# Optimization experiments

Measured on AMD Instinct MI355X. Metric: run time of the kernel, lower is better.

The kernel has to match this reference:

```python
import jax, jax.numpy as jnp
import numpy as np

UNITS = 1024
N_FEATURES = 128
OUT_STEPS = 32
EPS = 1e-7


def _lstm_cell(x, h, c, W, U, b):
    # Keras LSTMCell: gates ordered i, f, g(candidate), o
    z = x @ W + h @ U + b  # [B, 4U]
    i, f, g, o = jnp.split(z, 4, axis=-1)
    i = jax.nn.sigmoid(i)
    f = jax.nn.sigmoid(f)
    g = jnp.tanh(g)
    o = jax.nn.sigmoid(o)
    c_new = f * c + i * g
    h_new = o * jnp.tanh(c_new)
    return h_new, c_new


def setup_inputs() -> dict:
    key = jax.random.key(0)
    ks = jax.random.split(key, 12)
    B, T, F, U = 512, 64, N_FEATURES, UNITS
    s = lambda fan_in: 1.0 / np.sqrt(fan_in)
    return {
        "inputs": jax.random.normal(ks[0], (B, T, F), jnp.float32),
        "mean": jax.random.normal(ks[1], (F,), jnp.float32) * 0.1,
        "var": jax.random.uniform(ks[2], (F,), jnp.float32, 0.5, 1.5),
        "W1": jax.random.normal(ks[3], (F, 4 * U), jnp.float32) * s(F),
        "U1": jax.random.normal(ks[4], (U, 4 * U), jnp.float32) * s(U),
        "b1": jnp.zeros((4 * U,), jnp.float32),
        "W2": jax.random.normal(ks[5], (U, 4 * U), jnp.float32) * s(U),
        "U2": jax.random.normal(ks[6], (U, 4 * U), jnp.float32) * s(U),
        "b2": jnp.zeros((4 * U,), jnp.float32),
        "Wd": jax.random.normal(ks[7], (U, F), jnp.float32) * s(U),
        "bd": jnp.zeros((F,), jnp.float32),
    }


def reference(inputs, mean, var, W1, U1, b1, W2, U2, b2, Wd, bd):
    B = inputs.shape[0]
    inv_std = jax.lax.rsqrt(var + EPS)
    # NOTE: original call() normalizes, then warmup() normalizes AGAIN -- faithful.
    x = (inputs - mean) * inv_std
    x = (x - mean) * inv_std

    # --- warmup: RNN(cell1) over input sequence, return last h and state ---
    h0 = jnp.zeros((B, UNITS), x.dtype)
    c0 = jnp.zeros((B, UNITS), x.dtype)

    def warm_step(carry, xt):
        h, c = carry
        h, c = _lstm_cell(xt, h, c, W1, U1, b1)
        return (h, c), None

    (h, c), _ = jax.lax.scan(warm_step, (h0, c0), jnp.swapaxes(x, 0, 1))
    pred0 = h @ Wd + bd  # [B, F]

    def ar_step(carry, _):
        pred, h, c = carry
        h, c = _lstm_cell(pred, h, c, W1, U1, b1)
        h, c = _lstm_cell(h, h, c, W2, U2, b2)
        pred = h @ Wd + bd
        return (pred, h, c), pred

    _, preds = jax.lax.scan(ar_step, (pred0, h, c), None, length=OUT_STEPS - 1)
    preds = jnp.concatenate([pred0[None], preds], axis=0)  # [out_steps, B, F]
    return jnp.transpose(preds, (1, 0, 2))  # [B, out_steps, F]
```

## Files before the change

kernel.cpp:

```cpp
#include <hip/hip_runtime.h>
#include <stdint.h>

#define NB 512
#define NT 64
#define NF 128
#define NU 1024
#define NG 4096
#define NS 32

typedef __attribute__((ext_vector_type(8))) short short8;
typedef __attribute__((ext_vector_type(4))) float f32x4;
typedef __attribute__((ext_vector_type(4))) unsigned int u32x4;

__device__ __forceinline__ float sigm(float x) { return 1.0f / (1.0f + __expf(-x)); }
__device__ __forceinline__ float tanh_f(float x) {
  float ax = fabsf(x);
  float e = __expf(2.0f * ax);
  float t = 1.0f - 2.0f / (e + 1.0f);
  return copysignf(t, x);
}
__device__ __forceinline__ unsigned short f2bf(float f) {
  union { float f; unsigned u; } v; v.f = f;
  unsigned r = v.u + 0x7fffu + ((v.u >> 16) & 1u);
  return (unsigned short)(r >> 16);
}

__device__ __forceinline__ void coh_store_bf16(unsigned short* p, unsigned v) {
  asm volatile("global_store_short %0, %1, off sc0 sc1" :: "v"(p), "v"(v) : "memory");
}

__device__ __forceinline__ void gbar_grp(unsigned* gf, int u_blk, unsigned gen) {
  __syncthreads();
  if (threadIdx.x == 0)
    __hip_atomic_store(gf + u_blk, gen, __ATOMIC_RELAXED, __HIP_MEMORY_SCOPE_AGENT);
  if (threadIdx.x < 16) {
    while (__hip_atomic_load(gf + threadIdx.x, __ATOMIC_RELAXED, __HIP_MEMORY_SCOPE_AGENT) < gen)
      __builtin_amdgcn_s_sleep(1);
  }
  __syncthreads();
}

template <int KX>
__device__ __forceinline__ void do_step(
    const unsigned short* __restrict__ hIn,
    const unsigned short* __restrict__ Bp,
    const unsigned short* __restrict__ Xp,
    const unsigned short* __restrict__ W1p,
    int tstep, f32x4 bA, f32x4 (&cst)[2],
    unsigned short* __restrict__ hOut, unsigned short* __restrict__ hOut2,
    unsigned short* lds,
    int r0, int u0, int kh, int wu, int lr, int g4, int ucol, int tid)
{
  constexpr int ROWE = NU + KX;

  {
    u32x4 t[8];
    const unsigned short* src[8];
    int loff[8];
#pragma unroll
    for (int it = 0; it < 8; ++it) {
      int i = tid + it * 512;
      int r = i >> 7, cb = i & 127;
      src[it] = hIn + (size_t)(r0 + r) * NU + cb * 8;
      loff[it] = r * (ROWE * 2) + ((cb * 16) ^ ((r & 7) << 4));
    }
#pragma unroll
    for (int it = 0; it < 8; ++it)
      asm volatile("global_load_dwordx4 %0, %1, off sc0 sc1" : "=v"(t[it]) : "v"(src[it]));
    if constexpr (KX > 0) {
      int r = tid >> 4, cb = tid & 15;
      u32x4 vx = *(const u32x4*)(Xp + ((size_t)tstep * NB + (r0 + r)) * NF + cb * 8);
      int ox = r * (ROWE * 2) + ((NU * 2 + cb * 16) ^ ((r & 7) << 4));
      asm volatile("s_waitcnt vmcnt(0)" ::: "memory");
      __builtin_amdgcn_sched_barrier(0);
#pragma unroll
      for (int it = 0; it < 8; ++it) *(u32x4*)((char*)lds + loff[it]) = t[it];
      *(u32x4*)((char*)lds + ox) = vx;
    } else {
      asm volatile("s_waitcnt vmcnt(0)" ::: "memory");
      __builtin_amdgcn_sched_barrier(0);
#pragma unroll
      for (int it = 0; it < 8; ++it) *(u32x4*)((char*)lds + loff[it]) = t[it];
    }
  }
  __syncthreads();

  f32x4 acc[4][2];
#pragma unroll
  for (int g = 0; g < 4; ++g)
#pragma unroll
    for (int rt = 0; rt < 2; ++rt) acc[g][rt] = (f32x4){0.f, 0.f, 0.f, 0.f};

  const char* ldsb = (const char*)lds;
  const int arow0 = lr * (ROWE * 2);
  const int arow1 = (16 + lr) * (ROWE * 2);
  const int axor = (lr & 7) << 4;
  const int kcb = kh * 16;

  short8 nb[2][4];
  {
    size_t b0 = ((size_t)(kcb * 4 + g4) * NG + ucol) * 8;
    size_t b1 = ((size_t)((kcb + 1) * 4 + g4) * NG + ucol) * 8;
#pragma unroll
    for (int g = 0; g < 4; ++g) {
      nb[0][g] = *(const short8*)(Bp + b0 + (size_t)g * NU * 8);
      nb[1][g] = *(const short8*)(Bp + b1 + (size_t)g * NU * 8);
    }
  }
#pragma unroll 4
  for (int kc = 0; kc < 16; ++kc) {
    short8 bb[4];
#pragma unroll
    for (int g = 0; g < 4; ++g) bb[g] = nb[kc & 1][g];
    if (kc < 14) {
      size_t base = ((size_t)((kcb + kc + 2) * 4 + g4) * NG + ucol) * 8;
#pragma unroll
      for (int g = 0; g < 4; ++g) nb[kc & 1][g] = *(const short8*)(Bp + base + (size_t)g * NU * 8);
    }
    int kb = ((kcb + kc) * 64 + g4 * 16) ^ axor;
    short8 a0 = *(const short8*)(ldsb + arow0 + kb);
    short8 a1 = *(const short8*)(ldsb + arow1 + kb);
#pragma unroll
    for (int g = 0; g < 4; ++g) {
      acc[g][0] = __builtin_amdgcn_mfma_f32_16x16x32_bf16(a0, bb[g], acc[g][0], 0, 0, 0);
      acc[g][1] = __builtin_amdgcn_mfma_f32_16x16x32_bf16(a1, bb[g], acc[g][1], 0, 0, 0);
    }
  }
  if constexpr (KX > 0) {
#pragma unroll
    for (int kc = kh * 2; kc < kh * 2 + 2; ++kc) {
      int kb = (NU * 2 + kc * 64 + g4 * 16) ^ axor;
      short8 a0 = *(const short8*)(ldsb + arow0 + kb);
      short8 a1 = *(const short8*)(ldsb + arow1 + kb);
      size_t base = ((size_t)(kc * 4 + g4) * NG + ucol) * 8;
      short8 bb[4];
#pragma unroll
      for (int g = 0; g < 4; ++g) bb[g] = *(const short8*)(W1p + base + (size_t)g * NU * 8);
#pragma unroll
      for (int g = 0; g < 4; ++g) {
        acc[g][0] = __builtin_amdgcn_mfma_f32_16x16x32_bf16(a0, bb[g], acc[g][0], 0, 0, 0);
        acc[g][1] = __builtin_amdgcn_mfma_f32_16x16x32_bf16(a1, bb[g], acc[g][1], 0, 0, 0);
      }
    }
  }

  __syncthreads();
  float* red = (float*)lds;
  const int l = (g4 << 4) | lr;
  if (kh == 1) {
#pragma unroll
    for (int g = 0; g < 4; ++g)
#pragma unroll
      for (int rt = 0; rt < 2; ++rt)
        *(f32x4*)(red + (size_t)(((wu * 8) + (g * 2 + rt)) * 64 + l) * 4) = acc[g][rt];
  }
  __syncthreads();
  if (kh == 0) {
#pragma unroll
    for (int g = 0; g < 4; ++g)
#pragma unroll
      for (int rt = 0; rt < 2; ++rt)
        acc[g][rt] += *(const f32x4*)(red + (size_t)(((wu * 8) + (g * 2 + rt)) * 64 + l) * 4);

#pragma unroll
    for (int rt = 0; rt < 2; ++rt) {
#pragma unroll
      for (int j = 0; j < 4; ++j) {
        int r = r0 + rt * 16 + g4 * 4 + j;
        size_t idx = (size_t)r * NU + ucol;
        float iv = sigm(acc[0][rt][j] + bA[0]);
        float fv = sigm(acc[1][rt][j] + bA[1]);
        float gv = tanh_f(acc[2][rt][j] + bA[2]);
        float ov = sigm(acc[3][rt][j] + bA[3]);
        float cN = fv * cst[rt][j] + iv * gv;
        cst[rt][j] = cN;
        unsigned hv = f2bf(ov * tanh_f(cN));
        coh_store_bf16(hOut + idx, hv);
        if (hOut2) coh_store_bf16(hOut2 + idx, hv);
      }
    }
  }
}

__global__ __launch_bounds__(512, 2) void lstm_seq(
    const unsigned short* __restrict__ U1p, const unsigned short* __restrict__ U1pp,
    const unsigned short* __restrict__ W2U2p, const unsigned short* __restrict__ W1p,
    const unsigned short* __restrict__ x2,
    const float* __restrict__ b1, const float* __restrict__ b1p, const float* __restrict__ b2,
    unsigned short* __restrict__ h0, unsigned short* __restrict__ h1,
    unsigned short* __restrict__ hist, unsigned* __restrict__ flags)
{
  extern __shared__ unsigned short lds[];
  const int bid = blockIdx.x;
  const int xcd = bid & 7, slot = bid >> 3;
  const int u_blk = xcd * 2 + (slot >> 4);
  const int m_blk = slot & 15;
  const int r0 = m_blk * 32, u0 = u_blk * 64;
  const int tid = threadIdx.x;
  const int w = tid >> 6, kh = w >> 2, wu = w & 3;
  const int lr = tid & 15, g4 = (tid >> 4) & 3;
  const int ucol = u0 + wu * 16 + lr;
  const size_t HS = (size_t)NB * NU;
  unsigned* gf = flags + m_blk * 64;

  f32x4 bW, bC1, bC2;
#pragma unroll
  for (int g = 0; g < 4; ++g) {
    bW[g]  = b1 [g * NU + ucol];
    bC1[g] = b1p[g * NU + ucol];
    bC2[g] = b2 [g * NU + ucol];
  }
  f32x4 cst[2];
  cst[0] = (f32x4){0.f, 0.f, 0.f, 0.f};
  cst[1] = (f32x4){0.f, 0.f, 0.f, 0.f};

  unsigned gen = 0;
  for (int t = 0; t < NT; ++t) {
    const unsigned short* hi = (t & 1) ? h1 : h0;
    unsigned short* ho = (t & 1) ? h0 : h1;
    do_step<NF>(hi, U1p, x2, W1p, t, bW, cst, ho, (t == NT - 1) ? hist : nullptr,
                lds, r0, u0, kh, wu, lr, g4, ucol, tid);
    gbar_grp(gf, u_blk, ++gen);
  }
  for (int s = 0; s < NS - 1; ++s) {
    do_step<0>(h0, U1pp, nullptr, nullptr, 0, bC1, cst, h1, nullptr,
               lds, r0, u0, kh, wu, lr, g4, ucol, tid);
    gbar_grp(gf, u_blk, ++gen);
    do_step<0>(h1, W2U2p, nullptr, nullptr, 0, bC2, cst, h0, hist + (size_t)(s + 1) * HS,
               lds, r0, u0, kh, wu, lr, g4, ucol, tid);
    if (s < NS - 2) gbar_grp(gf, u_blk, ++gen);
  }
}

__global__ __launch_bounds__(256, 2) void pred_gemm(
    const unsigned short* __restrict__ H,
    const unsigned short* __restrict__ Wdp,
    const float* __restrict__ bd, float* __restrict__ out)
{
  __shared__ unsigned short lds[32 * NU];
  const int tid = threadIdx.x;
  const int r0 = blockIdx.x * 32;
  for (int i = tid; i < 32 * 128; i += 256) {
    int r = i >> 7, cb = i & 127;
    uint4 v = *(const uint4*)(H + (size_t)(r0 + r) * NU + cb * 8);
    int off = r * 2048 + ((cb * 16) ^ ((r & 7) << 4));
    *(uint4*)((char*)lds + off) = v;
  }
  __syncthreads();
  const int w = tid >> 6, l = tid & 63, lr = l & 15, g4 = l >> 4;
  f32x4 acc[2][2];
#pragma unroll
  for (int a = 0; a < 2; ++a)
#pragma unroll
    for (int c = 0; c < 2; ++c) acc[a][c] = (f32x4){0.f, 0.f, 0.f, 0.f};
  const char* ldsb = (const char*)lds;
  const int arow0 = lr * 2048, arow1 = (16 + lr) * 2048, axor = (lr & 7) << 4;
  const int col0 = w * 32 + lr;
#pragma unroll 4
  for (int kc = 0; kc < 32; ++kc) {
    int kb = (kc * 64 + g4 * 16) ^ axor;
    short8 a0 = *(const short8*)(ldsb + arow0 + kb);
    short8 a1 = *(const short8*)(ldsb + arow1 + kb);
    size_t base = ((size_t)(kc * 4 + g4) * NF) * 8;
    short8 w0 = *(const short8*)(Wdp + base + (size_t)col0 * 8);
    short8 w1 = *(const short8*)(Wdp + base + (size_t)(col0 + 16) * 8);
    acc[0][0] = __builtin_amdgcn_mfma_f32_16x16x32_bf16(a0, w0, acc[0][0], 0, 0, 0);
    acc[1][0] = __builtin_amdgcn_mfma_f32_16x16x32_bf16(a1, w0, acc[1][0], 0, 0, 0);
    acc[0][1] = __builtin_amdgcn_mfma_f32_16x16x32_bf16(a0, w1, acc[0][1], 0, 0, 0);
    acc[1][1] = __builtin_amdgcn_mfma_f32_16x16x32_bf16(a1, w1, acc[1][1], 0, 0, 0);
  }
#pragma unroll
  for (int rt = 0; rt < 2; ++rt)
#pragma unroll
    for (int ct = 0; ct < 2; ++ct)
#pragma unroll
      for (int j = 0; j < 4; ++j) {
        int r = r0 + rt * 16 + g4 * 4 + j;
        int s = r >> 9, bb = r & 511;
        int f = w * 32 + ct * 16 + lr;
        out[((size_t)bb * NS + s) * NF + f] = acc[rt][ct][j] + bd[f];
      }
}

__global__ void prep_x(const float* __restrict__ in, const float* __restrict__ mean,
                       const float* __restrict__ var, unsigned short* __restrict__ x2) {
  int i = (blockIdx.x * 256 + threadIdx.x) * 4;
  int f = i & 127;
  int bt = i >> 7;
  int b = bt >> 6, t = bt & 63;
  float4 v = *(const float4*)(in + i);
  float vv[4] = {v.x, v.y, v.z, v.w};
  unsigned short o[4] __attribute__((aligned(8)));
#pragma unroll
  for (int j = 0; j < 4; ++j) {
    float inv = rsqrtf(var[f + j] + 1e-7f);
    float s = inv * inv;
    float m2 = mean[f + j] * (s + inv);
    o[j] = f2bf(vv[j] * s - m2);
  }
  *(uint2*)(x2 + (((size_t)t * NB + b) << 7) + f) = *(const uint2*)o;
}

__global__ void prep_pack(const float* __restrict__ A, const float* __restrict__ A2,
                          unsigned short* __restrict__ P, int N) {
  int idx = blockIdx.x * 256 + threadIdx.x;
  int kg = idx / N, c = idx - kg * N;
  unsigned short o[8] __attribute__((aligned(16)));
#pragma unroll
  for (int j = 0; j < 8; ++j) {
    size_t e = (size_t)(kg * 8 + j) * N + c;
    float vv = A[e];
    if (A2) vv += A2[e];
    o[j] = f2bf(vv);
  }
  *(uint4*)(P + (size_t)idx * 8) = *(const uint4*)o;
}

__global__ __launch_bounds__(256) void prep_u1pp(
    const float* __restrict__ U1, const float* __restrict__ Wd,
    const float* __restrict__ W1, unsigned short* __restrict__ P) {
  __shared__ float wd[8][NF];
  const int kg = blockIdx.x >> 4;
  const int c = ((blockIdx.x & 15) << 8) + threadIdx.x;
  for (int i = threadIdx.x; i < 8 * NF; i += 256)
    wd[i >> 7][i & 127] = Wd[(size_t)(kg * 8 + (i >> 7)) * NF + (i & 127)];
  __syncthreads();
  float a[8];
#pragma unroll
  for (int j = 0; j < 8; ++j) a[j] = U1[(size_t)(kg * 8 + j) * NG + c];
#pragma unroll 8
  for (int m = 0; m < NF; ++m) {
    float w1v = W1[(size_t)m * NG + c];
#pragma unroll
    for (int j = 0; j < 8; ++j) a[j] += wd[j][m] * w1v;
  }
  unsigned short o[8] __attribute__((aligned(16)));
#pragma unroll
  for (int j = 0; j < 8; ++j) o[j] = f2bf(a[j]);
  *(uint4*)(P + (size_t)(kg * NG + c) * 8) = *(const uint4*)o;
}

__global__ void prep_wdp(const float* __restrict__ Wd, unsigned short* __restrict__ P) {
  int idx = blockIdx.x * 256 + threadIdx.x;
  int kg = idx >> 7, f = idx & 127;
  unsigned short o[8] __attribute__((aligned(16)));
#pragma unroll
  for (int j = 0; j < 8; ++j) o[j] = f2bf(Wd[(size_t)(kg * 8 + j) * NF + f]);
  *(uint4*)(P + (size_t)idx * 8) = *(const uint4*)o;
}

__global__ void prep_b1p(const float* __restrict__ b1, const float* __restrict__ bd,
                         const float* __restrict__ W1, float* __restrict__ o) {
  int c = blockIdx.x * 256 + threadIdx.x;
  float acc = b1[c];
#pragma unroll 8
  for (int m = 0; m < NF; ++m) acc += bd[m] * W1[(size_t)m * NG + c];
  o[c] = acc;
}

extern "C" void kernel_launch(void* const* d_in, const int* in_sizes, int n_in,
                              void* d_out, int out_size, void* d_ws, size_t ws_size,
                              hipStream_t stream) {
  const float* inputs = (const float*)d_in[0];
  const float* mean = (const float*)d_in[1];
  const float* var  = (const float*)d_in[2];
  const float* W1   = (const float*)d_in[3];
  const float* U1   = (const float*)d_in[4];
  const float* b1   = (const float*)d_in[5];
  const float* W2   = (const float*)d_in[6];
  const float* U2   = (const float*)d_in[7];
  const float* b2   = (const float*)d_in[8];
  const float* Wd   = (const float*)d_in[9];
  const float* bd   = (const float*)d_in[10];
  float* out = (float*)d_out;
  char* ws = (char*)d_ws;

  size_t off = 0;
  auto alloc = [&](size_t bytes) { char* p = ws + off; off += (bytes + 255) & ~255ull; return p; };
  unsigned short* h0    = (unsigned short*)alloc((size_t)NB * NU * 2);
  unsigned short* h1    = (unsigned short*)alloc((size_t)NB * NU * 2);
  unsigned short* hist  = (unsigned short*)alloc((size_t)NS * NB * NU * 2);
  unsigned short* x2    = (unsigned short*)alloc((size_t)NB * NT * NF * 2);
  unsigned short* U1p   = (unsigned short*)alloc((size_t)NU * NG * 2);
  unsigned short* U1pp  = (unsigned short*)alloc((size_t)NU * NG * 2);
  unsigned short* W2U2p = (unsigned short*)alloc((size_t)NU * NG * 2);
  unsigned short* W1p   = (unsigned short*)alloc((size_t)NF * NG * 2);
  unsigned short* Wdp   = (unsigned short*)alloc((size_t)NU * NF * 2);
  float* b1p            = (float*)alloc((size_t)NG * 4);
  unsigned* flags       = (unsigned*)alloc(16 * 64 * 4);

  hipMemsetAsync(h0, 0, (size_t)NB * NU * 2, stream);
  hipMemsetAsync(flags, 0, 16 * 64 * 4, stream);

  prep_x   <<<(NB * NT * NF) / 1024, 256, 0, stream>>>(inputs, mean, var, x2);
  prep_pack<<<(NU / 8) * NG / 256, 256, 0, stream>>>(U1, nullptr, U1p, NG);
  prep_u1pp<<<(NU / 8) * NG / 256, 256, 0, stream>>>(U1, Wd, W1, U1pp);
  prep_pack<<<(NU / 8) * NG / 256, 256, 0, stream>>>(W2, U2, W2U2p, NG);
  prep_pack<<<(NF / 8) * NG / 256, 256, 0, stream>>>(W1, nullptr, W1p, NG);
  prep_wdp <<<(NU / 8) * NF / 256, 256, 0, stream>>>(Wd, Wdp);
  prep_b1p <<<NG / 256, 256, 0, stream>>>(b1, bd, W1, b1p);

  lstm_seq<<<256, 512, 98304, stream>>>(U1p, U1pp, W2U2p, W1p, x2,
                                        b1, b1p, b2, h0, h1, hist, flags);

  pred_gemm<<<(NS * NB) / 32, 256, 0, stream>>>(hist, Wdp, bd, out);
}
```

Before: 1.208 ms.

## Split grid barrier so weight prefetch overlaps the wait for peers

The group barrier is split into a signal at the end of each step and a wait at the start of the next. The first six k-chunks of recurrent weights, which do not depend on other blocks, are issued before spinning on peer flags, so weight fetch latency hides behind synchronisation. The weight prefetch ring also grows from double-buffered to six-deep with a fully unrolled k loop. The cost is higher register pressure, and the spin now sits after outstanding loads.

```diff
diff --git a/kernel.cpp b/kernel.cpp
--- a/kernel.cpp
+++ b/kernel.cpp
@@ -24,20 +24,10 @@
   unsigned r = v.u + 0x7fffu + ((v.u >> 16) & 1u);
   return (unsigned short)(r >> 16);
 }
+__device__ __forceinline__ short8 as_s8(u32x4 v) { return __builtin_bit_cast(short8, v); }
 
 __device__ __forceinline__ void coh_store_bf16(unsigned short* p, unsigned v) {
   asm volatile("global_store_short %0, %1, off sc0 sc1" :: "v"(p), "v"(v) : "memory");
-}
-
-__device__ __forceinline__ void gbar_grp(unsigned* gf, int u_blk, unsigned gen) {
-  __syncthreads();
-  if (threadIdx.x == 0)
-    __hip_atomic_store(gf + u_blk, gen, __ATOMIC_RELAXED, __HIP_MEMORY_SCOPE_AGENT);
-  if (threadIdx.x < 16) {
-    while (__hip_atomic_load(gf + threadIdx.x, __ATOMIC_RELAXED, __HIP_MEMORY_SCOPE_AGENT) < gen)
-      __builtin_amdgcn_s_sleep(1);
-  }
-  __syncthreads();
 }
 
 template <int KX>
@@ -49,9 +39,28 @@
     int tstep, f32x4 bA, f32x4 (&cst)[2],
     unsigned short* __restrict__ hOut, unsigned short* __restrict__ hOut2,
     unsigned short* lds,
+    unsigned* gf, int u_blk, unsigned gen,
     int r0, int u0, int kh, int wu, int lr, int g4, int ucol, int tid)
 {
   constexpr int ROWE = NU + KX;
+  const int kcb = kh * 16;
+
+  u32x4 nb[6][4];
+#pragma unroll
+  for (int p = 0; p < 6; ++p) {
+    size_t base = ((size_t)((kcb + p) * 4 + g4) * NG + ucol) * 8;
+#pragma unroll
+    for (int g = 0; g < 4; ++g) {
+      const unsigned short* gp = Bp + base + (size_t)g * NU * 8;
+      asm volatile("global_load_dwordx4 %0, %1, off" : "=v"(nb[p][g]) : "v"(gp));
+    }
+  }
+
+  if (threadIdx.x < 16) {
+    while (__hip_atomic_load(gf + threadIdx.x, __ATOMIC_RELAXED, __HIP_MEMORY_SCOPE_AGENT) < gen)
+      __builtin_amdgcn_s_sleep(1);
+  }
+  __syncthreads();
 
   {
     u32x4 t[8];
@@ -95,27 +104,17 @@
   const int arow0 = lr * (ROWE * 2);
   const int arow1 = (16 + lr) * (ROWE * 2);
   const int axor = (lr & 7) << 4;
-  const int kcb = kh * 16;
-
-  short8 nb[2][4];
-  {
-    size_t b0 = ((size_t)(kcb * 4 + g4) * NG + ucol) * 8;
-    size_t b1 = ((size_t)((kcb + 1) * 4 + g4) * NG + ucol) * 8;
-#pragma unroll
-    for (int g = 0; g < 4; ++g) {
-      nb[0][g] = *(const short8*)(Bp + b0 + (size_t)g * NU * 8);
-      nb[1][g] = *(const short8*)(Bp + b1 + (size_t)g * NU * 8);
-    }
-  }
-#pragma unroll 4
+
+#pragma unroll
   for (int kc = 0; kc < 16; ++kc) {
     short8 bb[4];
 #pragma unroll
-    for (int g = 0; g < 4; ++g) bb[g] = nb[kc & 1][g];
-    if (kc < 14) {
-      size_t base = ((size_t)((kcb + kc + 2) * 4 + g4) * NG + ucol) * 8;
-#pragma unroll
-      for (int g = 0; g < 4; ++g) nb[kc & 1][g] = *(const short8*)(Bp + base + (size_t)g * NU * 8);
+    for (int g = 0; g < 4; ++g) bb[g] = as_s8(nb[kc % 6][g]);
+    if (kc < 10) {
+      size_t base = ((size_t)((kcb + kc + 6) * 4 + g4) * NG + ucol) * 8;
+#pragma unroll
+      for (int g = 0; g < 4; ++g)
+        nb[kc % 6][g] = *(const u32x4*)(Bp + base + (size_t)g * NU * 8);
     }
     int kb = ((kcb + kc) * 64 + g4 * 16) ^ axor;
     short8 a0 = *(const short8*)(ldsb + arow0 + kb);
@@ -180,6 +179,10 @@
       }
     }
   }
+
+  __syncthreads();
+  if (threadIdx.x == 0)
+    __hip_atomic_store(gf + u_blk, gen + 1, __ATOMIC_RELAXED, __HIP_MEMORY_SCOPE_AGENT);
 }
 
 __global__ __launch_bounds__(512, 2) void lstm_seq(
@@ -219,16 +222,16 @@
     const unsigned short* hi = (t & 1) ? h1 : h0;
     unsigned short* ho = (t & 1) ? h0 : h1;
     do_step<NF>(hi, U1p, x2, W1p, t, bW, cst, ho, (t == NT - 1) ? hist : nullptr,
-                lds, r0, u0, kh, wu, lr, g4, ucol, tid);
-    gbar_grp(gf, u_blk, ++gen);
+                lds, gf, u_blk, gen, r0, u0, kh, wu, lr, g4, ucol, tid);
+    ++gen;
   }
   for (int s = 0; s < NS - 1; ++s) {
     do_step<0>(h0, U1pp, nullptr, nullptr, 0, bC1, cst, h1, nullptr,
-               lds, r0, u0, kh, wu, lr, g4, ucol, tid);
-    gbar_grp(gf, u_blk, ++gen);
+               lds, gf, u_blk, gen, r0, u0, kh, wu, lr, g4, ucol, tid);
+    ++gen;
     do_step<0>(h1, W2U2p, nullptr, nullptr, 0, bC2, cst, h0, hist + (size_t)(s + 1) * HS,
-               lds, r0, u0, kh, wu, lr, g4, ucol, tid);
-    if (s < NS - 2) gbar_grp(gf, u_blk, ++gen);
+               lds, gf, u_blk, gen, r0, u0, kh, wu, lr, g4, ucol, tid);
+    ++gen;
   }
 }
 
```

Measured after the change: 2.856 ms. +136.4%, slower.
